# Kernel tuning notes

Measured on AMD Instinct MI355X. Metric: run time of the kernel, lower is better.

## Reference

```python
import jax, jax.numpy as jnp
import numpy as np

L, B, S, D, H, DK, F = 4, 2, 1024, 1024, 16, 64, 4096
EPS = 1e-5  # torch BatchNorm1d default eps


def setup_inputs() -> dict:
    key = jax.random.key(0)
    ks = iter(jax.random.split(key, 64))
    def nrm(shape, scale=0.02):
        return jax.random.normal(next(ks), shape, dtype=jnp.float32) * scale
    inp = {"x": jax.random.normal(next(ks), (B, S, D), dtype=jnp.float32)}
    for i in (1, 2):  # 1 = masked self-attn, 2 = second (unmasked) self-attn
        inp[f"Wq{i}"] = nrm((L, H, D, DK)); inp[f"bq{i}"] = nrm((L, H, DK))
        inp[f"Wk{i}"] = nrm((L, H, D, DK)); inp[f"bk{i}"] = nrm((L, H, DK))
        inp[f"Wv{i}"] = nrm((L, H, D, DK)); inp[f"bv{i}"] = nrm((L, H, DK))
        inp[f"Wo{i}"] = nrm((L, H * DK, D)); inp[f"bo{i}"] = nrm((L, D))
    for i in (1, 2, 3):
        inp[f"g{i}"] = 1.0 + nrm((L, D), 0.1)
        inp[f"be{i}"] = nrm((L, D), 0.1)
    inp["W1"] = nrm((L, D, F)); inp["bf1"] = nrm((L, F))
    inp["W2"] = nrm((L, F, D)); inp["bf2"] = nrm((L, D))
    inp["mask_idx"] = 512
    return inp


def _bn(x, g, b):
    # torch BatchNorm1d(model_dim) on a (B,S,D) tensor: channel axis is 1 (S==D),
    # training mode -> batch statistics over axes (0, 2), biased variance.
    mean = jnp.mean(x, axis=(0, 2), keepdims=True)
    var = jnp.var(x, axis=(0, 2), keepdims=True)
    return g[None, :, None] * (x - mean) * jax.lax.rsqrt(var + EPS) + b[None, :, None]


def _mha(x, Wq, bq, Wk, bk, Wv, bv, Wo, bo, mask_idx):
    # All heads batched into one einsum (same math as the per-head Python loop).
    Bx, Sx, _ = x.shape
    Hh, _, dk = Wq.shape
    q = jnp.einsum('bsd,hdk->bhsk', x, Wq) + bq[None, :, None, :]
    k = jnp.einsum('bsd,hdk->bhsk', x, Wk) + bk[None, :, None, :]
    v = jnp.einsum('bsd,hdk->bhsk', x, Wv) + bv[None, :, None, :]
    s = jnp.einsum('bhsk,bhtk->bhst', q, k) / jnp.sqrt(jnp.asarray(dk, x.dtype))
    if mask_idx is not None:
        # attention_weights[..., mask_idx:] = -inf  (static prefix mask, not causal)
        s = s.at[..., mask_idx:].set(-jnp.inf)
    w = jax.nn.softmax(s, axis=-1)
    a = jnp.einsum('bhst,bhtk->bhsk', w, v)
    a = jnp.transpose(a, (0, 2, 1, 3)).reshape(Bx, Sx, Hh * dk)  # concat heads
    return a @ Wo + bo


def _decoder(x, p, mask_idx):
    def block(h, pl):
        x1 = h + _mha(h, pl['Wq1'], pl['bq1'], pl['Wk1'], pl['bk1'],
                      pl['Wv1'], pl['bv1'], pl['Wo1'], pl['bo1'], mask_idx)
        x1 = _bn(x1, pl['g1'], pl['be1'])
        # note: residual from the block input h, attention over x1 (as in source)
        y = h + _mha(x1, pl['Wq2'], pl['bq2'], pl['Wk2'], pl['bk2'],
                     pl['Wv2'], pl['bv2'], pl['Wo2'], pl['bo2'], None)
        y = _bn(y, pl['g2'], pl['be2'])
        hid = jax.nn.relu(y @ pl['W1'] + pl['bf1'])
        out = x1 + hid @ pl['W2'] + pl['bf2']  # residual from x1 (as in source)
        return _bn(out, pl['g3'], pl['be3']), None
    out, _ = jax.lax.scan(block, x, p)
    return out


def reference(x, Wq1, bq1, Wk1, bk1, Wv1, bv1, Wo1, bo1,
              Wq2, bq2, Wk2, bk2, Wv2, bv2, Wo2, bo2,
              g1, be1, g2, be2, g3, be3, W1, bf1, W2, bf2, mask_idx):
    p = dict(Wq1=Wq1, bq1=bq1, Wk1=Wk1, bk1=bk1, Wv1=Wv1, bv1=bv1, Wo1=Wo1, bo1=bo1,
             Wq2=Wq2, bq2=bq2, Wk2=Wk2, bk2=bk2, Wv2=Wv2, bv2=bv2, Wo2=Wo2, bo2=bo2,
             g1=g1, be1=be1, g2=g2, be2=be2, g3=g3, be3=be3,
             W1=W1, bf1=bf1, W2=W2, bf2=bf2)
    return _decoder(x, p, int(mask_idx))
```

## Files before the change

### kernel.cpp

```cpp
#include <hip/hip_runtime.h>
#include <cstdint>
#include <cstddef>

typedef unsigned short u16;
typedef unsigned int u32;

typedef __bf16 bf16x8 __attribute__((ext_vector_type(8)));
typedef float f32x4 __attribute__((ext_vector_type(4)));
typedef unsigned short u16x8 __attribute__((ext_vector_type(8)));

__device__ __forceinline__ float bf2f(u16 v) { return __builtin_bit_cast(float, (u32)v << 16); }
__device__ __forceinline__ u16 f2bf(float f) {
    u32 u = __builtin_bit_cast(u32, f);
    u += 0x7fffu + ((u >> 16) & 1u);
    return (u16)(u >> 16);
}
__device__ __forceinline__ bf16x8 ld8(const u16* p) {
    return __builtin_bit_cast(bf16x8, *(const uint4*)p);
}
__device__ __forceinline__ void glds16(const u16* g, u16* l) {
    __builtin_amdgcn_global_load_lds((const __attribute__((address_space(1))) void*)g,
                                     (__attribute__((address_space(3))) void*)l, 16, 0, 0);
}

struct B4 { const float* p[4]; };

__global__ __launch_bounds__(256) void conv_f2b(const float* __restrict__ src,
                                                u16* __restrict__ dst)
{
    int idx = blockIdx.x * 256 + threadIdx.x;
    float4 v = ((const float4*)src)[idx];
    uint2 o;
    o.x = (u32)f2bf(v.x) | ((u32)f2bf(v.y) << 16);
    o.y = (u32)f2bf(v.z) | ((u32)f2bf(v.w) << 16);
    ((uint2*)dst)[idx] = o;
}

template <int BM, int BN>
__global__ __launch_bounds__(256) void gemm_bt(
    const u16* __restrict__ A, int lda,
    const u16* __restrict__ Bt, int ldb, int nbs,
    B4 bias,
    const u16* __restrict__ Rres,
    u16* __restrict__ C, int crow, int cbatch, int chead,
    int K, int relu)
{
    constexpr int WM = BM / 2, WN = BN / 2, FM = WM / 16, FN = WN / 16;
    __shared__ __align__(16) u16 Ald[2][BM * 64];
    __shared__ __align__(16) u16 Bld[2][BN * 64];
    const int tid = threadIdx.x;
    const int w = tid >> 6, lane = tid & 63;
    const int qd = lane >> 4, r = lane & 15;
    const int wr = w >> 1, wc = w & 1;
    const int m0 = blockIdx.y * BM, n0 = blockIdx.x * BN;
    const int srow = lane >> 3;
    const int scol = ((lane ^ (lane >> 3)) & 7) * 8;

    auto stage = [&](int buf, int k0) {
#pragma unroll
        for (int ii = 0; ii < BM / 32; ++ii) {
            int rbase = w * (BM / 4) + ii * 8;
            glds16(A + (long)(m0 + rbase + srow) * lda + k0 + scol,
                   &Ald[buf][rbase * 64]);
        }
#pragma unroll
        for (int ii = 0; ii < BN / 32; ++ii) {
            int nbase = w * (BN / 4) + ii * 8;
            int ng = n0 + nbase + srow;
            glds16(Bt + (long)(ng >> 6) * nbs + (long)(ng & 63) * ldb + k0 + scol,
                   &Bld[buf][nbase * 64]);
        }
    };

    f32x4 acc[FM][FN] = {};
    const int nt = K >> 6;

    stage(0, 0);
    __syncthreads();

    for (int t = 0; t < nt; ++t) {
        const int cur = t & 1;
        if (t + 1 < nt) stage(cur ^ 1, (t + 1) << 6);
#pragma unroll
        for (int s = 0; s < 2; ++s) {
            bf16x8 af[FM], bb[FN];
#pragma unroll
            for (int fm = 0; fm < FM; ++fm) {
                int row = wr * WM + fm * 16 + r;
                int blk = ((s << 2) | qd) ^ (r & 7);
                af[fm] = ld8(&Ald[cur][row * 64 + blk * 8]);
            }
#pragma unroll
            for (int fn = 0; fn < FN; ++fn) {
                int row = wc * WN + fn * 16 + r;
                int blk = ((s << 2) | qd) ^ (r & 7);
                bb[fn] = ld8(&Bld[cur][row * 64 + blk * 8]);
            }
#pragma unroll
            for (int fm = 0; fm < FM; ++fm)
#pragma unroll
                for (int fn = 0; fn < FN; ++fn)
                    acc[fm][fn] = __builtin_amdgcn_mfma_f32_16x16x32_bf16(af[fm], bb[fn],
                                                                          acc[fm][fn], 0, 0, 0);
        }
        __syncthreads();
    }

#pragma unroll
    for (int fm = 0; fm < FM; ++fm) {
#pragma unroll
        for (int fn = 0; fn < FN; ++fn) {
            int ng = n0 + wc * WN + fn * 16 + r;
            float bs = bias.p[ng >> 10][ng & 1023];
            int naddr = (ng >> 6) * chead + (ng & 63);
#pragma unroll
            for (int j = 0; j < 4; ++j) {
                int mg = m0 + wr * WM + fm * 16 + qd * 4 + j;
                int caddr = (mg & 1023) * crow + (mg >> 10) * cbatch + naddr;
                float v = acc[fm][fn][j] + bs;
                if (Rres) v += bf2f(Rres[caddr]);
                if (relu) v = fmaxf(v, 0.f);
                C[caddr] = f2bf(v);
            }
        }
    }
}

__global__ __launch_bounds__(256) void vtrans(const u16* __restrict__ src,
                                              u16* __restrict__ dst)
{
    __shared__ u16 tl[32][68];
    const long boff = (long)blockIdx.y * 65536;
    const int s0 = blockIdx.x * 32;
    const int c = threadIdx.x & 63, r4 = threadIdx.x >> 6;
#pragma unroll
    for (int i = 0; i < 8; ++i)
        tl[r4 + 4 * i][c] = src[boff + (long)(s0 + r4 + 4 * i) * 64 + c];
    __syncthreads();
    const int cs = threadIdx.x & 31, rs = threadIdx.x >> 5;
#pragma unroll
    for (int i = 0; i < 8; ++i)
        dst[boff + (long)(rs + 8 * i) * 1024 + s0 + cs] = tl[cs][rs + 8 * i];
}

__global__ __launch_bounds__(256) void attn_kernel(
    const u16* __restrict__ Q, const u16* __restrict__ K,
    const u16* __restrict__ V, u16* __restrict__ O,
    const int* __restrict__ maskp)
{
    constexpr int PST = 1032;
    __shared__ __align__(16) u16 P[16 * PST];
    __shared__ float ssm[4][16];
    const int tid = threadIdx.x;
    const int w = tid >> 6, lane = tid & 63;
    const int qd = lane >> 4, r = lane & 15;
    const int qt = blockIdx.x, bh = blockIdx.y;
    const int b = bh >> 4, h = bh & 15;
    const long base = (long)h * 131072 + (long)b * 65536;

    int mi = maskp ? *maskp : 1024;
    mi = mi < 0 ? 0 : (mi > 1024 ? 1024 : mi);
    const int nt = (mi + 15) >> 4;
    const int KC = nt ? ((nt * 16 + 31) & ~31) : 0;

    if (KC > nt * 16) {
        int row = tid >> 4, col = nt * 16 + (tid & 15);
        P[row * PST + col] = 0;
    }

    bf16x8 aq0 = ld8(&Q[base + (qt * 16 + r) * 64 + qd * 8]);
    bf16x8 aq1 = ld8(&Q[base + (qt * 16 + r) * 64 + 32 + qd * 8]);

    float sm[4] = {0.f, 0.f, 0.f, 0.f};
#pragma unroll
    for (int it = 0; it < 16; ++it) {
        int t = w + it * 4;
        if (t < nt) {
            const u16* kb = &K[base + (t * 16 + r) * 64 + qd * 8];
            f32x4 acc = {};
            acc = __builtin_amdgcn_mfma_f32_16x16x32_bf16(aq0, ld8(kb), acc, 0, 0, 0);
            acc = __builtin_amdgcn_mfma_f32_16x16x32_bf16(aq1, ld8(kb + 32), acc, 0, 0, 0);
            int col = t * 16 + r;
            bool valid = (col < mi);
#pragma unroll
            for (int j = 0; j < 4; ++j) {
                float p = valid ? __expf(fminf(acc[j] * 0.125f, 60.f)) : 0.f;
                sm[j] += p;
                P[(qd * 4 + j) * PST + col] = f2bf(p);
            }
        }
    }

#pragma unroll
    for (int d = 1; d < 16; d <<= 1)
#pragma unroll
        for (int j = 0; j < 4; ++j) sm[j] += __shfl_xor(sm[j], d);
    if (r == 0) {
#pragma unroll
        for (int j = 0; j < 4; ++j) ssm[w][qd * 4 + j] = sm[j];
    }
    __syncthreads();

    float scale[4];
#pragma unroll
    for (int j = 0; j < 4; ++j) {
        int row = qd * 4 + j;
        float gs = ssm[0][row] + ssm[1][row] + ssm[2][row] + ssm[3][row];
        scale[j] = 1.f / fmaxf(gs, 1e-30f);
    }

    f32x4 o = {};
    const u16* vb = &V[base + (long)(w * 16 + r) * 1024];
    for (int kk = 0; kk < KC; kk += 32) {
        bf16x8 pa = ld8(&P[r * PST + kk + qd * 8]);
        bf16x8 vv = ld8(&vb[kk + qd * 8]);
        o = __builtin_amdgcn_mfma_f32_16x16x32_bf16(pa, vv, o, 0, 0, 0);
    }
#pragma unroll
    for (int j = 0; j < 4; ++j) {
        int s = qt * 16 + qd * 4 + j;
        O[(long)(b * 1024 + s) * 1024 + h * 64 + w * 16 + r] = f2bf(o[j] * scale[j]);
    }
}

__global__ __launch_bounds__(256) void bn_kernel(
    const u16* __restrict__ X, u16* __restrict__ Y, float* __restrict__ Yf,
    const float* __restrict__ g, const float* __restrict__ be)
{
    __shared__ float red[8];
    const int s = blockIdx.x, tid = threadIdx.x;
    const long b0 = (long)s * 1024, b1 = (long)(1024 + s) * 1024;
    uint2 a0 = *(const uint2*)&X[b0 + tid * 4];
    uint2 a1 = *(const uint2*)&X[b1 + tid * 4];
    float xs[8];
    xs[0] = bf2f((u16)a0.x); xs[1] = bf2f((u16)(a0.x >> 16));
    xs[2] = bf2f((u16)a0.y); xs[3] = bf2f((u16)(a0.y >> 16));
    xs[4] = bf2f((u16)a1.x); xs[5] = bf2f((u16)(a1.x >> 16));
    xs[6] = bf2f((u16)a1.y); xs[7] = bf2f((u16)(a1.y >> 16));
    float s1 = 0.f, s2 = 0.f;
#pragma unroll
    for (int j = 0; j < 8; ++j) { s1 += xs[j]; s2 += xs[j] * xs[j]; }
    for (int o = 32; o; o >>= 1) { s1 += __shfl_down(s1, o); s2 += __shfl_down(s2, o); }
    if ((tid & 63) == 0) { red[(tid >> 6) * 2] = s1; red[(tid >> 6) * 2 + 1] = s2; }
    __syncthreads();
    float S1 = red[0] + red[2] + red[4] + red[6];
    float S2 = red[1] + red[3] + red[5] + red[7];
    float mean = S1 * (1.f / 2048.f);
    float var = fmaxf(S2 * (1.f / 2048.f) - mean * mean, 0.f);
    float gs = g[s] * rsqrtf(var + 1e-5f);
    float bs = be[s];
    float y[8];
#pragma unroll
    for (int j = 0; j < 8; ++j) y[j] = (xs[j] - mean) * gs + bs;
    if (Yf) {
        *(float4*)&Yf[b0 + tid * 4] = make_float4(y[0], y[1], y[2], y[3]);
        *(float4*)&Yf[b1 + tid * 4] = make_float4(y[4], y[5], y[6], y[7]);
    } else {
        *(uint2*)&Y[b0 + tid * 4] = make_uint2(
            (u32)f2bf(y[0]) | ((u32)f2bf(y[1]) << 16),
            (u32)f2bf(y[2]) | ((u32)f2bf(y[3]) << 16));
        *(uint2*)&Y[b1 + tid * 4] = make_uint2(
            (u32)f2bf(y[4]) | ((u32)f2bf(y[5]) << 16),
            (u32)f2bf(y[6]) | ((u32)f2bf(y[7]) << 16));
    }
}

struct TA { const float* s[10]; u16* d[10]; };

__global__ __launch_bounds__(256) void transpose_all(TA ta)
{
    __shared__ u16 tl[32][33];
    int id = blockIdx.x;
    const float* src; u16* dst; int Rr, Cc, tr, tc;
    if (id < 6144) {
        int wgt = id >> 10, rest = id & 1023;
        int head = rest >> 6, tile = rest & 63;
        tr = tile >> 1; tc = tile & 1; Rr = 1024; Cc = 64;
        src = ta.s[wgt] + head * 65536; dst = ta.d[wgt] + head * 65536;
    } else if (id < 8192) {
        int wgt = 6 + ((id - 6144) >> 10), rest = (id - 6144) & 1023;
        tr = rest >> 5; tc = rest & 31; Rr = 1024; Cc = 1024;
        src = ta.s[wgt]; dst = ta.d[wgt];
    } else if (id < 12288) {
        int rest = id - 8192;
        tr = rest >> 7; tc = rest & 127; Rr = 1024; Cc = 4096;
        src = ta.s[8]; dst = ta.d[8];
    } else {
        int rest = id - 12288;
        tr = rest >> 5; tc = rest & 31; Rr = 4096; Cc = 1024;
        src = ta.s[9]; dst = ta.d[9];
    }
    int r0 = tr * 32, c0 = tc * 32;
    int cl = threadIdx.x & 31, rl = threadIdx.x >> 5;
#pragma unroll
    for (int i = 0; i < 4; ++i)
        tl[rl + 8 * i][cl] = f2bf(src[(long)(r0 + rl + 8 * i) * Cc + c0 + cl]);
    __syncthreads();
#pragma unroll
    for (int i = 0; i < 4; ++i)
        dst[(long)(c0 + rl + 8 * i) * Rr + r0 + cl] = tl[cl][rl + 8 * i];
}

extern "C" void kernel_launch(void* const* d_in, const int* in_sizes, int n_in,
                              void* d_out, int out_size, void* d_ws, size_t ws_size,
                              hipStream_t stream)
{
    (void)in_sizes; (void)n_in; (void)out_size;
    const float* x   = (const float*)d_in[0];
    const float* Wq1 = (const float*)d_in[1];
    const float* bq1 = (const float*)d_in[2];
    const float* Wk1 = (const float*)d_in[3];
    const float* bk1 = (const float*)d_in[4];
    const float* Wv1 = (const float*)d_in[5];
    const float* bv1 = (const float*)d_in[6];
    const float* Wo1 = (const float*)d_in[7];
    const float* bo1 = (const float*)d_in[8];
    const float* Wq2 = (const float*)d_in[9];
    const float* bq2 = (const float*)d_in[10];
    const float* Wk2 = (const float*)d_in[11];
    const float* bk2 = (const float*)d_in[12];
    const float* Wv2 = (const float*)d_in[13];
    const float* bv2 = (const float*)d_in[14];
    const float* Wo2 = (const float*)d_in[15];
    const float* bo2 = (const float*)d_in[16];
    const float* g1  = (const float*)d_in[17];
    const float* be1 = (const float*)d_in[18];
    const float* g2  = (const float*)d_in[19];
    const float* be2 = (const float*)d_in[20];
    const float* g3  = (const float*)d_in[21];
    const float* be3 = (const float*)d_in[22];
    const float* W1  = (const float*)d_in[23];
    const float* bf1 = (const float*)d_in[24];
    const float* W2  = (const float*)d_in[25];
    const float* bf2 = (const float*)d_in[26];
    const int* maskp = (const int*)d_in[27];

    u16* ws = (u16*)d_ws;
    const size_t M1 = 1u << 20;
    u16* WT  = ws;
    u16* QKV = ws + 16 * M1;
    u16* Vt  = ws + 22 * M1;
    u16* Ab  = ws + 24 * M1;
    u16* X1  = ws + 26 * M1;
    u16* Yb  = ws + 28 * M1;
    u16* Hb  = ws + 30 * M1;
    u16* HID = ws + 32 * M1;
    u16* T2  = Ab;
    if (ws_size < (size_t)(40 * M1) * sizeof(u16)) return;

    dim3 blk(256);
    dim3 g64(16, 32);
    dim3 gqkv(48, 16);
    dim3 gF1(64, 16);
    dim3 gvt(32, 32);

    conv_f2b<<<dim3(2048), blk, 0, stream>>>(x, Hb);

    for (int l = 0; l < 4; ++l) {
        const u16* hin = Hb;

        TA ta;
        ta.s[0] = Wq1 + (size_t)l * M1;     ta.d[0] = WT + 0 * M1;
        ta.s[1] = Wk1 + (size_t)l * M1;     ta.d[1] = WT + 1 * M1;
        ta.s[2] = Wv1 + (size_t)l * M1;     ta.d[2] = WT + 2 * M1;
        ta.s[3] = Wq2 + (size_t)l * M1;     ta.d[3] = WT + 3 * M1;
        ta.s[4] = Wk2 + (size_t)l * M1;     ta.d[4] = WT + 4 * M1;
        ta.s[5] = Wv2 + (size_t)l * M1;     ta.d[5] = WT + 5 * M1;
        ta.s[6] = Wo1 + (size_t)l * M1;     ta.d[6] = WT + 6 * M1;
        ta.s[7] = Wo2 + (size_t)l * M1;     ta.d[7] = WT + 7 * M1;
        ta.s[8] = W1  + (size_t)l * 4 * M1; ta.d[8] = WT + 8 * M1;
        ta.s[9] = W2  + (size_t)l * 4 * M1; ta.d[9] = WT + 12 * M1;
        transpose_all<<<dim3(16384), blk, 0, stream>>>(ta);

        B4 bQKV1 = {{bq1 + l * 1024, bk1 + l * 1024, bv1 + l * 1024, nullptr}};
        gemm_bt<128, 64><<<gqkv, blk, 0, stream>>>(hin, 1024, WT + 0 * M1, 1024, 65536,
            bQKV1, nullptr, QKV, 64, 65536, 131072, 1024, 0);
        vtrans<<<gvt, blk, 0, stream>>>(QKV + 4 * M1, Vt);
        attn_kernel<<<dim3(64, 32), blk, 0, stream>>>(QKV, QKV + 2 * M1, Vt, Ab, maskp);
        B4 bO1 = {{bo1 + l * 1024, nullptr, nullptr, nullptr}};
        gemm_bt<64, 64><<<g64, blk, 0, stream>>>(Ab, 1024, WT + 6 * M1, 1024, 65536,
            bO1, hin, X1, 1024, 1048576, 64, 1024, 0);
        bn_kernel<<<dim3(1024), blk, 0, stream>>>(X1, X1, nullptr, g1 + l * 1024, be1 + l * 1024);

        B4 bQKV2 = {{bq2 + l * 1024, bk2 + l * 1024, bv2 + l * 1024, nullptr}};
        gemm_bt<128, 64><<<gqkv, blk, 0, stream>>>(X1, 1024, WT + 3 * M1, 1024, 65536,
            bQKV2, nullptr, QKV, 64, 65536, 131072, 1024, 0);
        vtrans<<<gvt, blk, 0, stream>>>(QKV + 4 * M1, Vt);
        attn_kernel<<<dim3(64, 32), blk, 0, stream>>>(QKV, QKV + 2 * M1, Vt, Ab, nullptr);
        B4 bO2 = {{bo2 + l * 1024, nullptr, nullptr, nullptr}};
        gemm_bt<64, 64><<<g64, blk, 0, stream>>>(Ab, 1024, WT + 7 * M1, 1024, 65536,
            bO2, hin, Yb, 1024, 1048576, 64, 1024, 0);
        bn_kernel<<<dim3(1024), blk, 0, stream>>>(Yb, Yb, nullptr, g2 + l * 1024, be2 + l * 1024);

        B4 bF1 = {{bf1 + l * 4096, bf1 + l * 4096 + 1024,
                   bf1 + l * 4096 + 2048, bf1 + l * 4096 + 3072}};
        gemm_bt<128, 64><<<gF1, blk, 0, stream>>>(Yb, 1024, WT + 8 * M1, 1024, 65536,
            bF1, nullptr, HID, 4096, 4194304, 64, 1024, 1);
        B4 bF2 = {{bf2 + l * 1024, nullptr, nullptr, nullptr}};
        gemm_bt<64, 64><<<g64, blk, 0, stream>>>(HID, 4096, WT + 12 * M1, 4096, 262144,
            bF2, X1, T2, 1024, 1048576, 64, 4096, 0);
        bn_kernel<<<dim3(1024), blk, 0, stream>>>(T2, Hb,
            (l == 3) ? (float*)d_out : nullptr, g3 + l * 1024, be3 + l * 1024);
    }
}
```

Before: 1.346 ms.

## Rewrite attention to keep P in registers with per-wave query tiles

The attention kernel now gives each wave its own 16 query rows across all 64 head dims. It computes S^T tiles so the exponentiated probabilities land directly in the MFMA A-operand layout, packed with v_cvt_pk_bf16_f32, and feeds them into the PV MFMAs in the same loop. This removes the shared-memory P buffer, the block-wide barrier and the cross-wave softmax-sum reduction. The grid becomes 1D with an XCD-aware mapping of blocks to (batch, head), meant to improve L2 reuse of K/V. In exchange, each wave now re-reads all of K and V for its own rows, which raises per-wave global load traffic.

```diff
diff --git a/kernel.cpp b/kernel.cpp
--- a/kernel.cpp
+++ b/kernel.cpp
@@ -7,7 +7,6 @@
 
 typedef __bf16 bf16x8 __attribute__((ext_vector_type(8)));
 typedef float f32x4 __attribute__((ext_vector_type(4)));
-typedef unsigned short u16x8 __attribute__((ext_vector_type(8)));
 
 __device__ __forceinline__ float bf2f(u16 v) { return __builtin_bit_cast(float, (u32)v << 16); }
 __device__ __forceinline__ u16 f2bf(float f) {
@@ -17,6 +16,11 @@
 }
 __device__ __forceinline__ bf16x8 ld8(const u16* p) {
     return __builtin_bit_cast(bf16x8, *(const uint4*)p);
+}
+__device__ __forceinline__ u32 cvtpk(float lo, float hi) {
+    u32 r;
+    asm("v_cvt_pk_bf16_f32 %0, %1, %2" : "=v"(r) : "v"(lo), "v"(hi));
+    return r;
 }
 __device__ __forceinline__ void glds16(const u16* g, u16* l) {
     __builtin_amdgcn_global_load_lds((const __attribute__((address_space(1))) void*)g,
@@ -148,79 +152,88 @@
     const u16* __restrict__ V, u16* __restrict__ O,
     const int* __restrict__ maskp)
 {
-    constexpr int PST = 1032;
-    __shared__ __align__(16) u16 P[16 * PST];
-    __shared__ float ssm[4][16];
     const int tid = threadIdx.x;
     const int w = tid >> 6, lane = tid & 63;
     const int qd = lane >> 4, r = lane & 15;
-    const int qt = blockIdx.x, bh = blockIdx.y;
+    const int bid = blockIdx.x;
+    const int xcd = bid & 7, slot = bid >> 3;
+    const int bh = xcd + 8 * (slot & 3);
+    const int qx = slot >> 2;
     const int b = bh >> 4, h = bh & 15;
     const long base = (long)h * 131072 + (long)b * 65536;
+    const int qrow0 = qx * 64 + w * 16;
 
     int mi = maskp ? *maskp : 1024;
     mi = mi < 0 ? 0 : (mi > 1024 ? 1024 : mi);
-    const int nt = (mi + 15) >> 4;
-    const int KC = nt ? ((nt * 16 + 31) & ~31) : 0;
-
-    if (KC > nt * 16) {
-        int row = tid >> 4, col = nt * 16 + (tid & 15);
-        P[row * PST + col] = 0;
-    }
-
-    bf16x8 aq0 = ld8(&Q[base + (qt * 16 + r) * 64 + qd * 8]);
-    bf16x8 aq1 = ld8(&Q[base + (qt * 16 + r) * 64 + 32 + qd * 8]);
-
-    float sm[4] = {0.f, 0.f, 0.f, 0.f};
-#pragma unroll
-    for (int it = 0; it < 16; ++it) {
-        int t = w + it * 4;
-        if (t < nt) {
-            const u16* kb = &K[base + (t * 16 + r) * 64 + qd * 8];
-            f32x4 acc = {};
-            acc = __builtin_amdgcn_mfma_f32_16x16x32_bf16(aq0, ld8(kb), acc, 0, 0, 0);
-            acc = __builtin_amdgcn_mfma_f32_16x16x32_bf16(aq1, ld8(kb + 32), acc, 0, 0, 0);
-            int col = t * 16 + r;
-            bool valid = (col < mi);
+    const int ntch = (mi + 31) >> 5;
+
+    bf16x8 aq0 = ld8(&Q[base + (qrow0 + r) * 64 + qd * 8]);
+    bf16x8 aq1 = ld8(&Q[base + (qrow0 + r) * 64 + 32 + qd * 8]);
+
+    f32x4 occ[4] = {};
+    float sm = 0.f;
+    const u16* kp = K + base + r * 64 + qd * 8;
+    const u16* vp = V + base + (long)r * 1024 + qd * 4;
+
+    for (int c = 0; c < ntch; ++c) {
+        const u16* kb = kp + c * 2048;
+        f32x4 s0 = {}, s1 = {};
+        s0 = __builtin_amdgcn_mfma_f32_16x16x32_bf16(ld8(kb),        aq0, s0, 0, 0, 0);
+        s0 = __builtin_amdgcn_mfma_f32_16x16x32_bf16(ld8(kb + 32),   aq1, s0, 0, 0, 0);
+        s1 = __builtin_amdgcn_mfma_f32_16x16x32_bf16(ld8(kb + 1024), aq0, s1, 0, 0, 0);
+        s1 = __builtin_amdgcn_mfma_f32_16x16x32_bf16(ld8(kb + 1056), aq1, s1, 0, 0, 0);
+
+        float p0[4], p1[4];
+        const int kbase = c * 32 + qd * 4;
+        if (kbase + 32 <= mi) {
 #pragma unroll
             for (int j = 0; j < 4; ++j) {
-                float p = valid ? __expf(fminf(acc[j] * 0.125f, 60.f)) : 0.f;
-                sm[j] += p;
-                P[(qd * 4 + j) * PST + col] = f2bf(p);
+                p0[j] = __expf(fminf(s0[j] * 0.125f, 60.f));
+                p1[j] = __expf(fminf(s1[j] * 0.125f, 60.f));
+                sm += p0[j] + p1[j];
             }
-        }
-    }
-
-#pragma unroll
-    for (int d = 1; d < 16; d <<= 1)
-#pragma unroll
-        for (int j = 0; j < 4; ++j) sm[j] += __shfl_xor(sm[j], d);
-    if (r == 0) {
-#pragma unroll
-        for (int j = 0; j < 4; ++j) ssm[w][qd * 4 + j] = sm[j];
-    }
-    __syncthreads();
-
-    float scale[4];
-#pragma unroll
-    for (int j = 0; j < 4; ++j) {
-        int row = qd * 4 + j;
-        float gs = ssm[0][row] + ssm[1][row] + ssm[2][row] + ssm[3][row];
-        scale[j] = 1.f / fmaxf(gs, 1e-30f);
-    }
-
-    f32x4 o = {};
-    const u16* vb = &V[base + (long)(w * 16 + r) * 1024];
-    for (int kk = 0; kk < KC; kk += 32) {
-        bf16x8 pa = ld8(&P[r * PST + kk + qd * 8]);
-        bf16x8 vv = ld8(&vb[kk + qd * 8]);
-        o = __builtin_amdgcn_mfma_f32_16x16x32_bf16(pa, vv, o, 0, 0, 0);
-    }
-#pragma unroll
-    for (int j = 0; j < 4; ++j) {
-        int s = qt * 16 + qd * 4 + j;
-        O[(long)(b * 1024 + s) * 1024 + h * 64 + w * 16 + r] = f2bf(o[j] * scale[j]);
-    }
+        } else {
+#pragma unroll
+            for (int j = 0; j < 4; ++j) {
+                p0[j] = (kbase + j < mi)      ? __expf(fminf(s0[j] * 0.125f, 60.f)) : 0.f;
+                p1[j] = (kbase + 16 + j < mi) ? __expf(fminf(s1[j] * 0.125f, 60.f)) : 0.f;
+                sm += p0[j] + p1[j];
+            }
+        }
+
+        uint4 pk;
+        pk.x = cvtpk(p0[0], p0[1]);
+        pk.y = cvtpk(p0[2], p0[3]);
+        pk.z = cvtpk(p1[0], p1[1]);
+        pk.w = cvtpk(p1[2], p1[3]);
+        bf16x8 pa = __builtin_bit_cast(bf16x8, pk);
+
+#pragma unroll
+        for (int c4 = 0; c4 < 4; ++c4) {
+            const u16* vb = vp + c4 * 16384 + c * 32;
+            uint2 lo = *(const uint2*)vb;
+            uint2 hi = *(const uint2*)(vb + 16);
+            uint4 vq = make_uint4(lo.x, lo.y, hi.x, hi.y);
+            occ[c4] = __builtin_amdgcn_mfma_f32_16x16x32_bf16(
+                pa, __builtin_bit_cast(bf16x8, vq), occ[c4], 0, 0, 0);
+        }
+    }
+
+    sm += __shfl_xor(sm, 16);
+    sm += __shfl_xor(sm, 32);
+    float scale = 1.f / fmaxf(sm, 1e-30f);
+    float scj[4];
+#pragma unroll
+    for (int j = 0; j < 4; ++j) scj[j] = __shfl(scale, qd * 4 + j);
+
+#pragma unroll
+    for (int c4 = 0; c4 < 4; ++c4)
+#pragma unroll
+        for (int j = 0; j < 4; ++j) {
+            int row = qrow0 + qd * 4 + j;
+            O[(long)(b * 1024 + row) * 1024 + h * 64 + c4 * 16 + r] =
+                f2bf(occ[c4][j] * scj[j]);
+        }
 }
 
 __global__ __launch_bounds__(256) void bn_kernel(
@@ -376,7 +389,7 @@
         gemm_bt<128, 64><<<gqkv, blk, 0, stream>>>(hin, 1024, WT + 0 * M1, 1024, 65536,
             bQKV1, nullptr, QKV, 64, 65536, 131072, 1024, 0);
         vtrans<<<gvt, blk, 0, stream>>>(QKV + 4 * M1, Vt);
-        attn_kernel<<<dim3(64, 32), blk, 0, stream>>>(QKV, QKV + 2 * M1, Vt, Ab, maskp);
+        attn_kernel<<<dim3(512), blk, 0, stream>>>(QKV, QKV + 2 * M1, Vt, Ab, maskp);
         B4 bO1 = {{bo1 + l * 1024, nullptr, nullptr, nullptr}};
         gemm_bt<64, 64><<<g64, blk, 0, stream>>>(Ab, 1024, WT + 6 * M1, 1024, 65536,
             bO1, hin, X1, 1024, 1048576, 64, 1024, 0);
@@ -386,7 +399,7 @@
         gemm_bt<128, 64><<<gqkv, blk, 0, stream>>>(X1, 1024, WT + 3 * M1, 1024, 65536,
             bQKV2, nullptr, QKV, 64, 65536, 131072, 1024, 0);
         vtrans<<<gvt, blk, 0, stream>>>(QKV + 4 * M1, Vt);
-        attn_kernel<<<dim3(64, 32), blk, 0, stream>>>(QKV, QKV + 2 * M1, Vt, Ab, nullptr);
+        attn_kernel<<<dim3(512), blk, 0, stream>>>(QKV, QKV + 2 * M1, Vt, Ab, nullptr);
         B4 bO2 = {{bo2 + l * 1024, nullptr, nullptr, nullptr}};
         gemm_bt<64, 64><<<g64, blk, 0, stream>>>(Ab, 1024, WT + 7 * M1, 1024, 65536,
             bO2, hin, Yb, 1024, 1048576, 64, 1024, 0);
```

Result: slower. 1.497 ms (+11.2%).
